# Performance work log

Measured on AMD Instinct MI355X. Metric: run time of the kernel, lower is better.

Reference implementation:

```python
import jax, jax.numpy as jnp
import numpy as np

N_NODES = 100000
N_EDGES = 1600000
IN_CH = 48
OUT_CH = 64
K = 2


def setup_inputs() -> dict:
    key = jax.random.key(0)
    k1, k2, k3, k4 = jax.random.split(key, 4)
    x = jax.random.normal(k1, (N_NODES, IN_CH), dtype=jnp.float32)
    edge_index = jax.random.randint(k2, (2, N_EDGES), 0, N_NODES, dtype=jnp.int64)
    W = jax.random.normal(k3, (IN_CH, OUT_CH), dtype=jnp.float32) * (1.0 / np.sqrt(IN_CH))
    b = jax.random.normal(k4, (OUT_CH,), dtype=jnp.float32) * 0.01
    return {"x": x, "edge_index": edge_index, "W": W, "b": b}


def _propagate(x, row, col):
    n = x.shape[0]
    # degree of each node counted over col (destination) indices
    deg = jax.ops.segment_sum(jnp.ones_like(col, dtype=x.dtype), col, num_segments=n)
    deg_inv_sqrt = jnp.where(deg > 0, jax.lax.rsqrt(jnp.where(deg > 0, deg, 1.0)), 0.0)
    norm = deg_inv_sqrt[row] * deg_inv_sqrt[col]  # [E]
    # gather-scale-scatter: out[col] += x[row] * norm
    msgs = x[row] * norm[:, None]  # [E, d]
    return jax.ops.segment_sum(msgs, col, num_segments=n)


def reference(x, edge_index, W, b):
    row, col = edge_index[0], edge_index[1]
    h = x
    for _ in range(K):
        h = _propagate(h, row, col)
    return h @ W + b
```

## Files before the change

### kernel.cpp

```cpp
#include <hip/hip_runtime.h>
#include <hip/hip_bf16.h>
#include <hip/hip_fp16.h>


#define N_NODES 100000
#define N_EDGES 1600000
#define IN_CH 48
#define OUT_CH 64
#define NBUCKETS 392
#define CAP 4608
#define EPB 2048
#define EPR 8
#define NBLK_EDGE 782
#define NBLK_BKT 391

__global__ void init_kernel(int* __restrict__ bucketCursor, int* __restrict__ binTotal) {
    int t = threadIdx.x;
    if (t < NBUCKETS) bucketCursor[t] = t * CAP;
    if (t < 64) binTotal[t] = 0;
}

__global__ void bucket_scatter_kernel(const int* __restrict__ row, const int* __restrict__ col,
                                      int* __restrict__ bucketCursor, int* __restrict__ edge_packed) {
    __shared__ int lh[NBUCKETS];
    __shared__ int lofs[NBUCKETS];
    __shared__ int lbase[NBUCKETS];
    __shared__ int stage[EPB];
    __shared__ unsigned short sbkt[EPB];
    __shared__ int wsum[4];
    int tid = threadIdx.x;
    int base = blockIdx.x * EPB;
    for (int i = tid; i < NBUCKETS; i += 256) lh[i] = 0;
    __syncthreads();
    #pragma unroll
    for (int k = 0; k < EPR; k++) {
        int e = base + k * 256 + tid;
        if (e < N_EDGES) atomicAdd(&lh[col[e] >> 8], 1);
    }
    __syncthreads();
    {
        int c0 = (tid < 196) ? lh[2 * tid] : 0;
        int c1 = (tid < 196) ? lh[2 * tid + 1] : 0;
        int s = c0 + c1;
        int incl = s;
        int lane = tid & 63, w = tid >> 6;
        #pragma unroll
        for (int o = 1; o < 64; o <<= 1) {
            int v = __shfl_up(incl, o, 64);
            if (lane >= o) incl += v;
        }
        if (lane == 63) wsum[w] = incl;
        __syncthreads();
        int wbase = 0;
        for (int k = 0; k < w; k++) wbase += wsum[k];
        int ex = wbase + incl - s;
        if (tid < 196) {
            lofs[2 * tid]     = ex;
            lofs[2 * tid + 1] = ex + c0;
        }
    }
    __syncthreads();
    for (int i = tid; i < NBUCKETS; i += 256) {
        int c = lh[i];
        if (c > 0) lbase[i] = atomicAdd(&bucketCursor[i], c);
        lh[i] = 0;
    }
    __syncthreads();
    #pragma unroll
    for (int k = 0; k < EPR; k++) {
        int e = base + k * 256 + tid;
        if (e < N_EDGES) {
            int c = col[e];
            int bkt = c >> 8;
            int r = atomicAdd(&lh[bkt], 1);
            int slot = lofs[bkt] + r;
            stage[slot] = (row[e] << 8) | (c & 255);
            sbkt[slot] = (unsigned short)bkt;
        }
    }
    __syncthreads();
    int total = (base + EPB <= N_EDGES) ? EPB : (N_EDGES - base);
    for (int i = tid; i < total; i += 256) {
        int bkt = sbkt[i];
        int dst = lbase[bkt] + (i - lofs[bkt]);
        if (dst < (bkt + 1) * CAP)
            edge_packed[dst] = stage[i];
    }
}

__global__ void fine_sort_kernel(const int* __restrict__ edge_packed,
                                 const int* __restrict__ bucketCursor,
                                 int* __restrict__ edge_src,
                                 int* __restrict__ deg, int* __restrict__ start,
                                 float* __restrict__ dis, int* __restrict__ binTotal) {
    __shared__ int fh[256];
    __shared__ int cur[256];
    __shared__ int bh[64];
    __shared__ int wsum2[4];
    int b = blockIdx.x;
    int t = threadIdx.x;
    int s0 = b * CAP;
    int s1 = min(bucketCursor[b], (b + 1) * CAP);
    int nodeBase = b << 8;
    fh[t] = 0;
    if (t < 64) bh[t] = 0;
    __syncthreads();
    for (int j = s0 + t; j < s1; j += 256)
        atomicAdd(&fh[edge_packed[j] & 255], 1);
    __syncthreads();
    int c = fh[t];
    int incl = c;
    {
        int sl = t & 63, sw = t >> 6;
        #pragma unroll
        for (int o = 1; o < 64; o <<= 1) {
            int v = __shfl_up(incl, o, 64);
            if (sl >= o) incl += v;
        }
        if (sl == 63) wsum2[sw] = incl;
        __syncthreads();
        int wbase = 0;
        for (int k = 0; k < sw; k++) wbase += wsum2[k];
        incl += wbase;
    }
    int ex = incl - c;
    int node = nodeBase + t;
    bool valid = (node < N_NODES);
    int d = c;
    float dv = (valid && d > 0) ? rsqrtf((float)d) : 0.0f;
    cur[t] = ex;
    if (valid) {
        deg[node] = d;
        start[node] = s0 + ex;
        dis[node] = dv;
        atomicAdd(&bh[min(d, 63)], 1);
    }
    __syncthreads();
    for (int j = s0 + t; j < s1; j += 256) {
        int rc = edge_packed[j];
        int p = atomicAdd(&cur[rc & 255], 1);
        edge_src[s0 + p] = rc >> 8;
    }
    __syncthreads();
    if (t < 64 && bh[t]) atomicAdd(&binTotal[t], bh[t]);
}

__global__ void scale_kernel(const float* __restrict__ x, const float* __restrict__ dis,
                             __half2* __restrict__ xs) {
    int g = blockIdx.x * 32 + (threadIdx.x >> 3);
    int c = (threadIdx.x & 7) * 3;
    float dd = dis[g];
    const float2* px = (const float2*)x + g * 24 + c;
    float2 v0 = px[0], v1 = px[1], v2 = px[2];
    __half2* q = xs + g * 24 + c;
    q[0] = __floats2half2_rn(v0.x * dd, v0.y * dd);
    q[1] = __floats2half2_rn(v1.x * dd, v1.y * dd);
    q[2] = __floats2half2_rn(v2.x * dd, v2.y * dd);
}

__global__ void binscan_kernel(const int* __restrict__ binTotal, int* __restrict__ binCursor) {
    if (threadIdx.x == 0) {
        int s = 0;
        for (int k = 63; k >= 0; k--) { binCursor[k] = s; s += binTotal[k]; }
    }
}

__global__ void order_kernel(const int* __restrict__ deg, const int* __restrict__ start,
                             const float* __restrict__ dis, int* __restrict__ binCursor,
                             int4* __restrict__ nodeinfo, int n) {
    __shared__ int lhist[64];
    __shared__ int lbase[64];
    int i = blockIdx.x * 256 + threadIdx.x;
    if (threadIdx.x < 64) lhist[threadIdx.x] = 0;
    __syncthreads();
    int bin = 0, myrank = 0;
    if (i < n) {
        bin = min(deg[i], 63);
        myrank = atomicAdd(&lhist[bin], 1);
    }
    __syncthreads();
    if (threadIdx.x < 64 && lhist[threadIdx.x] > 0)
        lbase[threadIdx.x] = atomicAdd(&binCursor[threadIdx.x], lhist[threadIdx.x]);
    __syncthreads();
    if (i < n)
        nodeinfo[lbase[bin] + myrank] = make_int4(i, start[i], deg[i], __float_as_int(dis[i]));
}

#define ACC6(v0, v1, v2) { \
    float2 u0 = __half22float2(v0), u1 = __half22float2(v1), u2 = __half22float2(v2); \
    a0 += u0.x; a1 += u0.y; a2 += u1.x; a3 += u1.y; a4 += u2.x; a5 += u2.y; }
#define ACC6B(v0, v1, v2) { \
    float2 u0 = __half22float2(v0), u1 = __half22float2(v1), u2 = __half22float2(v2); \
    b0 += u0.x; b1 += u0.y; b2 += u1.x; b3 += u1.y; b4 += u2.x; b5 += u2.y; }

#define DECLD8(P) __half2 P##00,P##01,P##02,P##10,P##11,P##12,P##20,P##21,P##22, \
                          P##30,P##31,P##32,P##40,P##41,P##42,P##50,P##51,P##52, \
                          P##60,P##61,P##62,P##70,P##71,P##72
#define DECLS8(S) int S##0,S##1,S##2,S##3,S##4,S##5,S##6,S##7
#define LOADSRC8(S) { S##0 = edge_src[j];   S##1 = edge_src[j+1]; \
                      S##2 = edge_src[j+2]; S##3 = edge_src[j+3]; \
                      S##4 = edge_src[j+4]; S##5 = edge_src[j+5]; \
                      S##6 = edge_src[j+6]; S##7 = edge_src[j+7]; j += 8; }
#define ISSUE8(P, S, basep) { \
    const __half2* q; \
    q = basep + S##0 * 24 + lane3; P##00 = q[0]; P##01 = q[1]; P##02 = q[2]; \
    q = basep + S##1 * 24 + lane3; P##10 = q[0]; P##11 = q[1]; P##12 = q[2]; \
    q = basep + S##2 * 24 + lane3; P##20 = q[0]; P##21 = q[1]; P##22 = q[2]; \
    q = basep + S##3 * 24 + lane3; P##30 = q[0]; P##31 = q[1]; P##32 = q[2]; \
    q = basep + S##4 * 24 + lane3; P##40 = q[0]; P##41 = q[1]; P##42 = q[2]; \
    q = basep + S##5 * 24 + lane3; P##50 = q[0]; P##51 = q[1]; P##52 = q[2]; \
    q = basep + S##6 * 24 + lane3; P##60 = q[0]; P##61 = q[1]; P##62 = q[2]; \
    q = basep + S##7 * 24 + lane3; P##70 = q[0]; P##71 = q[1]; P##72 = q[2]; }
#define CONSUME8(P) { ACC6(P##00,P##01,P##02); ACC6B(P##10,P##11,P##12); \
                      ACC6(P##20,P##21,P##22); ACC6B(P##30,P##31,P##32); \
                      ACC6(P##40,P##41,P##42); ACC6B(P##50,P##51,P##52); \
                      ACC6(P##60,P##61,P##62); ACC6B(P##70,P##71,P##72); }

#define GATHER_PIPELINE8(basep) { \
    int m = (e - s) >> 3; \
    DECLD8(A); DECLD8(B); \
    DECLS8(sa); DECLS8(sb); \
    if (m >= 2) { \
        LOADSRC8(sa); LOADSRC8(sb); \
        ISSUE8(A, sa, basep); \
        m -= 2; \
        while (m >= 2) { \
            LOADSRC8(sa); \
            ISSUE8(B, sb, basep); \
            CONSUME8(A); \
            LOADSRC8(sb); \
            ISSUE8(A, sa, basep); \
            CONSUME8(B); \
            m -= 2; \
        } \
        if (m == 1) { \
            LOADSRC8(sa); \
            ISSUE8(B, sb, basep); \
            CONSUME8(A); \
            ISSUE8(A, sa, basep); \
            CONSUME8(B); \
            CONSUME8(A); \
        } else { \
            ISSUE8(B, sb, basep); \
            CONSUME8(A); \
            CONSUME8(B); \
        } \
    } else if (m == 1) { \
        LOADSRC8(sa); \
        ISSUE8(A, sa, basep); \
        CONSUME8(A); \
    } \
    for (; j < e; ++j) { \
        const __half2* p0 = basep + edge_src[j] * 24 + lane3; \
        __half2 v00 = p0[0], v01 = p0[1], v02 = p0[2]; \
        ACC6(v00, v01, v02); \
    } \
    a0 += b0; a1 += b1; a2 += b2; a3 += b3; a4 += b4; a5 += b5; }

__global__ void __launch_bounds__(256, 4)
gather1_kernel(const __half2* __restrict__ xs,
               const int* __restrict__ edge_src,
               const int4* __restrict__ nodeinfo,
               __half2* __restrict__ h1) {
    int g = blockIdx.x * 32 + (threadIdx.x >> 3);
    int lane3 = (threadIdx.x & 7) * 3;
    int4 ni = nodeinfo[g];
    int node = ni.x, s = ni.y, e = s + ni.z;
    float dv = __int_as_float(ni.w);
    float a0 = 0, a1 = 0, a2 = 0, a3 = 0, a4 = 0, a5 = 0;
    float b0 = 0, b1 = 0, b2 = 0, b3 = 0, b4 = 0, b5 = 0;
    int j = s;
    GATHER_PIPELINE8(xs);
    float sc = dv * dv;
    __half2* q = h1 + node * 24 + lane3;
    q[0] = __floats2half2_rn(a0 * sc, a1 * sc);
    q[1] = __floats2half2_rn(a2 * sc, a3 * sc);
    q[2] = __floats2half2_rn(a4 * sc, a5 * sc);
}

__global__ void __launch_bounds__(256, 4)
gather2_gemm_kernel(const __half2* __restrict__ h1,
                    const int* __restrict__ edge_src,
                    const int4* __restrict__ nodeinfo,
                    const float* __restrict__ W,
                    const float* __restrict__ bias,
                    float* __restrict__ out) {
    __shared__ float sW[IN_CH * OUT_CH];
    __shared__ float sb[OUT_CH];
    __shared__ float sh[32][IN_CH + 1];

    for (int i = threadIdx.x; i < IN_CH * OUT_CH; i += 256) sW[i] = W[i];
    if (threadIdx.x < OUT_CH) sb[threadIdx.x] = bias[threadIdx.x];

    int nl = threadIdx.x >> 3;
    int lane = threadIdx.x & 7;
    int lane3 = lane * 3;
    int g = blockIdx.x * 32 + nl;
    int4 ni = nodeinfo[g];
    int node = ni.x, s = ni.y, e = s + ni.z;
    float dv = __int_as_float(ni.w);

    float a0 = 0, a1 = 0, a2 = 0, a3 = 0, a4 = 0, a5 = 0;
    float b0 = 0, b1 = 0, b2 = 0, b3 = 0, b4 = 0, b5 = 0;
    int j = s;
    GATHER_PIPELINE8(h1);
    int c0 = 6 * lane;
    sh[nl][c0 + 0] = a0 * dv;
    sh[nl][c0 + 1] = a1 * dv;
    sh[nl][c0 + 2] = a2 * dv;
    sh[nl][c0 + 3] = a3 * dv;
    sh[nl][c0 + 4] = a4 * dv;
    sh[nl][c0 + 5] = a5 * dv;
    __syncthreads();

    int j0 = lane * 8;
    float acc[8];
    #pragma unroll
    for (int i = 0; i < 8; i++) acc[i] = sb[j0 + i];
    for (int k = 0; k < IN_CH; k++) {
        float s0 = sh[nl][k];
        #pragma unroll
        for (int i = 0; i < 8; i++) acc[i] += s0 * sW[k * OUT_CH + j0 + i];
    }
    float4* o = (float4*)(out + (size_t)node * OUT_CH + j0);
    o[0] = make_float4(acc[0], acc[1], acc[2], acc[3]);
    o[1] = make_float4(acc[4], acc[5], acc[6], acc[7]);
}

extern "C" void kernel_launch(void* const* d_in, const int* in_sizes, int n_in,
                              void* d_out, int out_size, void* d_ws, size_t ws_size,
                              hipStream_t stream) {
    const float* x   = (const float*)d_in[0];
    const int*   ei  = (const int*)d_in[1];
    const float* W   = (const float*)d_in[2];
    const float* b   = (const float*)d_in[3];
    float* out = (float*)d_out;

    const int* row = ei;
    const int* col = ei + N_EDGES;

    int* ws_i = (int*)d_ws;
    int* bucketCursor = ws_i;
    int* binTotal     = ws_i + 512;
    int* binCursor    = ws_i + 576;
    int* deg          = ws_i + 1024;
    int* start        = ws_i + 101376;
    float* dis        = (float*)(ws_i + 201728);
    int4* nodeinfo    = (int4*)(ws_i + 302080);
    int* edge_packed  = ws_i + 703488;
    int* edge_src     = ws_i + 2509824;
    __half2* xs       = (__half2*)(ws_i + 4316160);
    __half2* h1       = (__half2*)(ws_i + 6716160);

    init_kernel<<<1, 512, 0, stream>>>(bucketCursor, binTotal);
    bucket_scatter_kernel<<<NBLK_EDGE, 256, 0, stream>>>(row, col, bucketCursor, edge_packed);
    fine_sort_kernel<<<NBLK_BKT, 256, 0, stream>>>(edge_packed, bucketCursor,
                                                   edge_src, deg, start, dis, binTotal);
    scale_kernel<<<N_NODES / 32, 256, 0, stream>>>(x, dis, xs);
    binscan_kernel<<<1, 64, 0, stream>>>(binTotal, binCursor);
    order_kernel<<<(N_NODES + 255) / 256, 256, 0, stream>>>(deg, start, dis, binCursor,
                                                            nodeinfo, N_NODES);

    gather1_kernel<<<N_NODES / 32, 256, 0, stream>>>(xs, edge_src, nodeinfo, h1);
    gather2_gemm_kernel<<<N_NODES / 32, 256, 0, stream>>>(h1, edge_src, nodeinfo, W, b, out);
}
```

Before: 229.3 us.

## Split fp16 features into three 16-channel slices to shrink gather working set

Features are stored as three separate 16-channel half-precision slices, and the first propagation runs as three kernel launches, one per slice. Each slice is 3.2 MB, so the random gather working set of each pass fits better in cache. The second gather loops over the three slices inside one kernel before the GEMM. Outputs and h1 are written with nontemporal stores. The cost is reading the edge list three times and having fewer bytes in flight per edge (one 4-byte load per lane instead of three).

```diff
diff --git a/kernel.cpp b/kernel.cpp
--- a/kernel.cpp
+++ b/kernel.cpp
@@ -13,6 +13,9 @@
 #define EPR 8
 #define NBLK_EDGE 782
 #define NBLK_BKT 391
+#define SLICE_H2 800000
+
+typedef __attribute__((ext_vector_type(4))) float fvec4;
 
 __global__ void init_kernel(int* __restrict__ bucketCursor, int* __restrict__ binTotal) {
     int t = threadIdx.x;
@@ -148,14 +151,14 @@
 __global__ void scale_kernel(const float* __restrict__ x, const float* __restrict__ dis,
                              __half2* __restrict__ xs) {
     int g = blockIdx.x * 32 + (threadIdx.x >> 3);
-    int c = (threadIdx.x & 7) * 3;
+    int l = threadIdx.x & 7;
     float dd = dis[g];
-    const float2* px = (const float2*)x + g * 24 + c;
-    float2 v0 = px[0], v1 = px[1], v2 = px[2];
-    __half2* q = xs + g * 24 + c;
-    q[0] = __floats2half2_rn(v0.x * dd, v0.y * dd);
-    q[1] = __floats2half2_rn(v1.x * dd, v1.y * dd);
-    q[2] = __floats2half2_rn(v2.x * dd, v2.y * dd);
+    const float2* px = (const float2*)x + g * 24;
+    #pragma unroll
+    for (int sl = 0; sl < 3; sl++) {
+        float2 v = px[sl * 8 + l];
+        xs[sl * SLICE_H2 + g * 8 + l] = __floats2half2_rn(v.x * dd, v.y * dd);
+    }
 }
 
 __global__ void binscan_kernel(const int* __restrict__ binTotal, int* __restrict__ binCursor) {
@@ -186,105 +189,83 @@
         nodeinfo[lbase[bin] + myrank] = make_int4(i, start[i], deg[i], __float_as_int(dis[i]));
 }
 
-#define ACC6(v0, v1, v2) { \
-    float2 u0 = __half22float2(v0), u1 = __half22float2(v1), u2 = __half22float2(v2); \
-    a0 += u0.x; a1 += u0.y; a2 += u1.x; a3 += u1.y; a4 += u2.x; a5 += u2.y; }
-#define ACC6B(v0, v1, v2) { \
-    float2 u0 = __half22float2(v0), u1 = __half22float2(v1), u2 = __half22float2(v2); \
-    b0 += u0.x; b1 += u0.y; b2 += u1.x; b3 += u1.y; b4 += u2.x; b5 += u2.y; }
-
-#define DECLD8(P) __half2 P##00,P##01,P##02,P##10,P##11,P##12,P##20,P##21,P##22, \
-                          P##30,P##31,P##32,P##40,P##41,P##42,P##50,P##51,P##52, \
-                          P##60,P##61,P##62,P##70,P##71,P##72
-#define DECLS8(S) int S##0,S##1,S##2,S##3,S##4,S##5,S##6,S##7
-#define LOADSRC8(S) { S##0 = edge_src[j];   S##1 = edge_src[j+1]; \
-                      S##2 = edge_src[j+2]; S##3 = edge_src[j+3]; \
-                      S##4 = edge_src[j+4]; S##5 = edge_src[j+5]; \
-                      S##6 = edge_src[j+6]; S##7 = edge_src[j+7]; j += 8; }
-#define ISSUE8(P, S, basep) { \
-    const __half2* q; \
-    q = basep + S##0 * 24 + lane3; P##00 = q[0]; P##01 = q[1]; P##02 = q[2]; \
-    q = basep + S##1 * 24 + lane3; P##10 = q[0]; P##11 = q[1]; P##12 = q[2]; \
-    q = basep + S##2 * 24 + lane3; P##20 = q[0]; P##21 = q[1]; P##22 = q[2]; \
-    q = basep + S##3 * 24 + lane3; P##30 = q[0]; P##31 = q[1]; P##32 = q[2]; \
-    q = basep + S##4 * 24 + lane3; P##40 = q[0]; P##41 = q[1]; P##42 = q[2]; \
-    q = basep + S##5 * 24 + lane3; P##50 = q[0]; P##51 = q[1]; P##52 = q[2]; \
-    q = basep + S##6 * 24 + lane3; P##60 = q[0]; P##61 = q[1]; P##62 = q[2]; \
-    q = basep + S##7 * 24 + lane3; P##70 = q[0]; P##71 = q[1]; P##72 = q[2]; }
-#define CONSUME8(P) { ACC6(P##00,P##01,P##02); ACC6B(P##10,P##11,P##12); \
-                      ACC6(P##20,P##21,P##22); ACC6B(P##30,P##31,P##32); \
-                      ACC6(P##40,P##41,P##42); ACC6B(P##50,P##51,P##52); \
-                      ACC6(P##60,P##61,P##62); ACC6B(P##70,P##71,P##72); }
-
-#define GATHER_PIPELINE8(basep) { \
-    int m = (e - s) >> 3; \
-    DECLD8(A); DECLD8(B); \
-    DECLS8(sa); DECLS8(sb); \
+#define DECLD4(P) __half2 P##0, P##1, P##2, P##3
+#define DECLS4(S) int S##0, S##1, S##2, S##3
+#define LOADSRC4(S) { S##0 = edge_src[j];   S##1 = edge_src[j+1]; \
+                      S##2 = edge_src[j+2]; S##3 = edge_src[j+3]; j += 4; }
+#define ISSUE4(P, S, basep) { \
+    P##0 = basep[S##0 * 8 + lane]; P##1 = basep[S##1 * 8 + lane]; \
+    P##2 = basep[S##2 * 8 + lane]; P##3 = basep[S##3 * 8 + lane]; }
+#define CONSUME4(P) { float2 u; \
+    u = __half22float2(P##0); a0 += u.x; a1 += u.y; \
+    u = __half22float2(P##1); b0 += u.x; b1 += u.y; \
+    u = __half22float2(P##2); a0 += u.x; a1 += u.y; \
+    u = __half22float2(P##3); b0 += u.x; b1 += u.y; }
+
+#define GATHER_PIPE(basep) { \
+    int m = (e - j) >> 2; \
+    DECLD4(A); DECLD4(B); \
+    DECLS4(sa); DECLS4(sb); \
     if (m >= 2) { \
-        LOADSRC8(sa); LOADSRC8(sb); \
-        ISSUE8(A, sa, basep); \
+        LOADSRC4(sa); LOADSRC4(sb); \
+        ISSUE4(A, sa, basep); \
         m -= 2; \
         while (m >= 2) { \
-            LOADSRC8(sa); \
-            ISSUE8(B, sb, basep); \
-            CONSUME8(A); \
-            LOADSRC8(sb); \
-            ISSUE8(A, sa, basep); \
-            CONSUME8(B); \
+            LOADSRC4(sa); \
+            ISSUE4(B, sb, basep); \
+            CONSUME4(A); \
+            LOADSRC4(sb); \
+            ISSUE4(A, sa, basep); \
+            CONSUME4(B); \
             m -= 2; \
         } \
         if (m == 1) { \
-            LOADSRC8(sa); \
-            ISSUE8(B, sb, basep); \
-            CONSUME8(A); \
-            ISSUE8(A, sa, basep); \
-            CONSUME8(B); \
-            CONSUME8(A); \
+            LOADSRC4(sa); \
+            ISSUE4(B, sb, basep); \
+            CONSUME4(A); \
+            ISSUE4(A, sa, basep); \
+            CONSUME4(B); \
+            CONSUME4(A); \
         } else { \
-            ISSUE8(B, sb, basep); \
-            CONSUME8(A); \
-            CONSUME8(B); \
+            ISSUE4(B, sb, basep); \
+            CONSUME4(A); \
+            CONSUME4(B); \
         } \
     } else if (m == 1) { \
-        LOADSRC8(sa); \
-        ISSUE8(A, sa, basep); \
-        CONSUME8(A); \
+        LOADSRC4(sa); \
+        ISSUE4(A, sa, basep); \
+        CONSUME4(A); \
     } \
     for (; j < e; ++j) { \
-        const __half2* p0 = basep + edge_src[j] * 24 + lane3; \
-        __half2 v00 = p0[0], v01 = p0[1], v02 = p0[2]; \
-        ACC6(v00, v01, v02); \
+        float2 u = __half22float2(basep[edge_src[j] * 8 + lane]); \
+        a0 += u.x; a1 += u.y; \
     } \
-    a0 += b0; a1 += b1; a2 += b2; a3 += b3; a4 += b4; a5 += b5; }
-
-__global__ void __launch_bounds__(256, 4)
-gather1_kernel(const __half2* __restrict__ xs,
-               const int* __restrict__ edge_src,
-               const int4* __restrict__ nodeinfo,
-               __half2* __restrict__ h1) {
+    a0 += b0; a1 += b1; }
+
+__global__ void gather1_kernel(const __half2* __restrict__ xsl,
+                               const int* __restrict__ edge_src,
+                               const int4* __restrict__ nodeinfo,
+                               __half2* __restrict__ h1l) {
     int g = blockIdx.x * 32 + (threadIdx.x >> 3);
-    int lane3 = (threadIdx.x & 7) * 3;
+    int lane = threadIdx.x & 7;
     int4 ni = nodeinfo[g];
-    int node = ni.x, s = ni.y, e = s + ni.z;
+    int node = ni.x;
+    int j = ni.y, e = j + ni.z;
     float dv = __int_as_float(ni.w);
-    float a0 = 0, a1 = 0, a2 = 0, a3 = 0, a4 = 0, a5 = 0;
-    float b0 = 0, b1 = 0, b2 = 0, b3 = 0, b4 = 0, b5 = 0;
-    int j = s;
-    GATHER_PIPELINE8(xs);
+    float a0 = 0, a1 = 0, b0 = 0, b1 = 0;
+    GATHER_PIPE(xsl);
     float sc = dv * dv;
-    __half2* q = h1 + node * 24 + lane3;
-    q[0] = __floats2half2_rn(a0 * sc, a1 * sc);
-    q[1] = __floats2half2_rn(a2 * sc, a3 * sc);
-    q[2] = __floats2half2_rn(a4 * sc, a5 * sc);
-}
-
-__global__ void __launch_bounds__(256, 4)
-gather2_gemm_kernel(const __half2* __restrict__ h1,
-                    const int* __restrict__ edge_src,
-                    const int4* __restrict__ nodeinfo,
-                    const float* __restrict__ W,
-                    const float* __restrict__ bias,
-                    float* __restrict__ out) {
+    __half2 hv = __floats2half2_rn(a0 * sc, a1 * sc);
+    __builtin_nontemporal_store(*(const unsigned int*)&hv,
+                                (unsigned int*)(h1l + node * 8 + lane));
+}
+
+__global__ void gather2_gemm_kernel(const __half2* __restrict__ h1,
+                                    const int* __restrict__ edge_src,
+                                    const int4* __restrict__ nodeinfo,
+                                    const float* __restrict__ W,
+                                    const float* __restrict__ bias,
+                                    float* __restrict__ out) {
     __shared__ float sW[IN_CH * OUT_CH];
     __shared__ float sb[OUT_CH];
     __shared__ float sh[32][IN_CH + 1];
@@ -294,23 +275,20 @@
 
     int nl = threadIdx.x >> 3;
     int lane = threadIdx.x & 7;
-    int lane3 = lane * 3;
     int g = blockIdx.x * 32 + nl;
     int4 ni = nodeinfo[g];
-    int node = ni.x, s = ni.y, e = s + ni.z;
+    int node = ni.x, st = ni.y, en = st + ni.z;
     float dv = __int_as_float(ni.w);
 
-    float a0 = 0, a1 = 0, a2 = 0, a3 = 0, a4 = 0, a5 = 0;
-    float b0 = 0, b1 = 0, b2 = 0, b3 = 0, b4 = 0, b5 = 0;
-    int j = s;
-    GATHER_PIPELINE8(h1);
-    int c0 = 6 * lane;
-    sh[nl][c0 + 0] = a0 * dv;
-    sh[nl][c0 + 1] = a1 * dv;
-    sh[nl][c0 + 2] = a2 * dv;
-    sh[nl][c0 + 3] = a3 * dv;
-    sh[nl][c0 + 4] = a4 * dv;
-    sh[nl][c0 + 5] = a5 * dv;
+    #pragma unroll
+    for (int sl = 0; sl < 3; sl++) {
+        const __half2* basep = h1 + sl * SLICE_H2;
+        float a0 = 0, a1 = 0, b0 = 0, b1 = 0;
+        int j = st, e = en;
+        GATHER_PIPE(basep);
+        sh[nl][sl * 16 + 2 * lane]     = a0 * dv;
+        sh[nl][sl * 16 + 2 * lane + 1] = a1 * dv;
+    }
     __syncthreads();
 
     int j0 = lane * 8;
@@ -322,9 +300,11 @@
         #pragma unroll
         for (int i = 0; i < 8; i++) acc[i] += s0 * sW[k * OUT_CH + j0 + i];
     }
-    float4* o = (float4*)(out + (size_t)node * OUT_CH + j0);
-    o[0] = make_float4(acc[0], acc[1], acc[2], acc[3]);
-    o[1] = make_float4(acc[4], acc[5], acc[6], acc[7]);
+    fvec4 o0 = {acc[0], acc[1], acc[2], acc[3]};
+    fvec4 o1 = {acc[4], acc[5], acc[6], acc[7]};
+    fvec4* o = (fvec4*)(out + (size_t)node * OUT_CH + j0);
+    __builtin_nontemporal_store(o0, o);
+    __builtin_nontemporal_store(o1, o + 1);
 }
 
 extern "C" void kernel_launch(void* const* d_in, const int* in_sizes, int n_in,
@@ -361,6 +341,8 @@
     order_kernel<<<(N_NODES + 255) / 256, 256, 0, stream>>>(deg, start, dis, binCursor,
                                                             nodeinfo, N_NODES);
 
-    gather1_kernel<<<N_NODES / 32, 256, 0, stream>>>(xs, edge_src, nodeinfo, h1);
+    for (int sl = 0; sl < 3; sl++)
+        gather1_kernel<<<N_NODES / 32, 256, 0, stream>>>(xs + sl * SLICE_H2, edge_src,
+                                                         nodeinfo, h1 + sl * SLICE_H2);
     gather2_gemm_kernel<<<N_NODES / 32, 256, 0, stream>>>(h1, edge_src, nodeinfo, W, b, out);
 }
```

Result: slower. 244.1 us (+6.5%).
